# Optimization experiments

Measured on AMD Instinct MI355X. Metric: run time of the kernel, lower is better.

Reference implementation:

```python
import jax, jax.numpy as jnp
import numpy as np

HID, HEADS, FFN = 2048, 16, 8192
HEAD_DIM = HID // HEADS
B, S = 2, 2048
EPS = 1e-5


def setup_inputs() -> dict:
    key = jax.random.key(0)
    ks = jax.random.split(key, 12)
    s = 0.02
    x = jax.random.normal(ks[0], (B, S, HID), dtype=jnp.float32)
    # additive causal mask: 0 on/below diagonal, -inf-like above
    neg = jnp.float32(-1e9)
    causal = jnp.where(jnp.tril(jnp.ones((S, S), dtype=bool)), 0.0, neg)
    mask = causal[None, None, :, :].astype(jnp.float32)
    return {
        "x": x,
        "mask": mask,
        "ln1_w": jnp.ones((HID,), jnp.float32),
        "ln1_b": jnp.zeros((HID,), jnp.float32),
        "q_w": jax.random.normal(ks[1], (HID, HID), jnp.float32) * s,
        "k_w": jax.random.normal(ks[2], (HID, HID), jnp.float32) * s,
        "v_w": jax.random.normal(ks[3], (HID, HID), jnp.float32) * s,
        "o_w": jax.random.normal(ks[4], (HID, HID), jnp.float32) * s,
        "ln2_w": jnp.ones((HID,), jnp.float32),
        "ln2_b": jnp.zeros((HID,), jnp.float32),
        "w1_w": jax.random.normal(ks[5], (FFN, HID), jnp.float32) * s,
        "w1_b": jnp.zeros((FFN,), jnp.float32),
        "wg_w": jax.random.normal(ks[6], (FFN, HID), jnp.float32) * s,
        "w2_w": jax.random.normal(ks[7], (HID, FFN), jnp.float32) * s,
        "w2_b": jnp.zeros((HID,), jnp.float32),
    }


def _layernorm(x, w, b):
    mu = jnp.mean(x, axis=-1, keepdims=True)
    var = jnp.mean(jnp.square(x - mu), axis=-1, keepdims=True)
    return (x - mu) * jax.lax.rsqrt(var + EPS) * w + b


def reference(x, mask, ln1_w, ln1_b, q_w, k_w, v_w, o_w,
              ln2_w, ln2_b, w1_w, w1_b, wg_w, w2_w, w2_b):
    b, s, _ = x.shape
    # --- attention sublayer ---
    h = _layernorm(x, ln1_w, ln1_b)
    def split_heads(y):  # [b,s,hid] -> [b,H,s,d]
        return y.reshape(b, s, HEADS, HEAD_DIM).transpose(0, 2, 1, 3)
    q = split_heads(h @ q_w.T)
    k = split_heads(h @ k_w.T)
    v = split_heads(h @ v_w.T)
    scale = jnp.sqrt(jnp.float32(HEAD_DIM))
    scores = jnp.einsum('bhqd,bhkd->bhqk', q, k) / scale + mask
    weights = jax.nn.softmax(scores, axis=-1)
    attn = jnp.einsum('bhqk,bhkd->bhqd', weights, v)
    attn = attn.transpose(0, 2, 1, 3).reshape(b, s, HID)
    x = x + attn @ o_w.T
    # --- SwiGLU FFN sublayer ---
    h2 = _layernorm(x, ln2_w, ln2_b)
    ff = jax.nn.silu(h2 @ w1_w.T + w1_b) * (h2 @ wg_w.T)
    x = x + ff @ w2_w.T + w2_b
    return x
```

## Files before the change

kernel.cpp:

```cpp
#include <hip/hip_runtime.h>
#include <cstdint>
#include <cstddef>

#define HIDN 2048
#define NROWS 4096
#define FFND 8192
#define SEQ 2048

typedef __attribute__((ext_vector_type(8))) __bf16 bf16x8;
typedef __attribute__((ext_vector_type(4))) float f32x4;

__device__ __forceinline__ unsigned short f2b(float f) {
    union { float f; unsigned u; } v; v.f = f;
    unsigned r = v.u + 0x7fffu + ((v.u >> 16) & 1u);
    return (unsigned short)(r >> 16);
}
__device__ __forceinline__ float b2f(unsigned short h) {
    union { unsigned u; float f; } v; v.u = ((unsigned)h) << 16; return v.f;
}
__device__ __forceinline__ void gload16(const void* g, void* lds) {
    __builtin_amdgcn_global_load_lds(
        (const __attribute__((address_space(1))) void*)g,
        (__attribute__((address_space(3))) void*)lds, 16, 0, 0);
}

__global__ __launch_bounds__(256) void f2b_kernel(const float* __restrict__ in,
                                                  unsigned short* __restrict__ out, int n4) {
    int i = blockIdx.x * 256 + threadIdx.x;
    if (i < n4) {
        float4 v = ((const float4*)in)[i];
        ushort4 o;
        o.x = f2b(v.x); o.y = f2b(v.y); o.z = f2b(v.z); o.w = f2b(v.w);
        ((ushort4*)out)[i] = o;
    }
}

__global__ __launch_bounds__(256) void ln_kernel(const float* __restrict__ x,
                                                 const float* __restrict__ w,
                                                 const float* __restrict__ b,
                                                 unsigned short* __restrict__ out) {
    int row = blockIdx.x, tid = threadIdx.x;
    const float4* xr = (const float4*)(x + (size_t)row * HIDN);
    float4 a0 = xr[tid], a1 = xr[tid + 256];
    float s  = a0.x + a0.y + a0.z + a0.w + a1.x + a1.y + a1.z + a1.w;
    float s2 = a0.x*a0.x + a0.y*a0.y + a0.z*a0.z + a0.w*a0.w
             + a1.x*a1.x + a1.y*a1.y + a1.z*a1.z + a1.w*a1.w;
#pragma unroll
    for (int i = 1; i < 64; i <<= 1) { s += __shfl_xor(s, i); s2 += __shfl_xor(s2, i); }
    __shared__ float red[8];
    if ((tid & 63) == 0) { red[tid >> 6] = s; red[4 + (tid >> 6)] = s2; }
    __syncthreads();
    s  = red[0] + red[1] + red[2] + red[3];
    s2 = red[4] + red[5] + red[6] + red[7];
    float mu  = s * (1.0f / HIDN);
    float var = s2 * (1.0f / HIDN) - mu * mu;
    float rstd = rsqrtf(var + 1e-5f);
    const float4* wv = (const float4*)w;
    const float4* bv = (const float4*)b;
    float4 w0 = wv[tid], w1 = wv[tid + 256], b0 = bv[tid], b1 = bv[tid + 256];
    ushort4 o0, o1;
    o0.x = f2b((a0.x - mu) * rstd * w0.x + b0.x);
    o0.y = f2b((a0.y - mu) * rstd * w0.y + b0.y);
    o0.z = f2b((a0.z - mu) * rstd * w0.z + b0.z);
    o0.w = f2b((a0.w - mu) * rstd * w0.w + b0.w);
    o1.x = f2b((a1.x - mu) * rstd * w1.x + b1.x);
    o1.y = f2b((a1.y - mu) * rstd * w1.y + b1.y);
    o1.z = f2b((a1.z - mu) * rstd * w1.z + b1.z);
    o1.w = f2b((a1.w - mu) * rstd * w1.w + b1.w);
    ushort4* orow = (ushort4*)(out + (size_t)row * HIDN);
    orow[tid] = o0; orow[tid + 256] = o1;
}

template <int EPI>
__global__ __launch_bounds__(256)
void gemm_bt(const unsigned short* __restrict__ A, const unsigned short* __restrict__ Bw,
             int M, int N, int K, int tiles_n, float scale,
             const float* __restrict__ bias, const float* __restrict__ resf,
             const unsigned short* __restrict__ aux,
             float* __restrict__ outf, unsigned short* __restrict__ outb) {
    __shared__ unsigned short Asm[128 * 32];
    __shared__ unsigned short Bsm[128 * 32];
    int tid = threadIdx.x;
    int wave = tid >> 6, lane = tid & 63;
    int lrow = lane & 15, quad = lane >> 4;
    int bm = blockIdx.x / tiles_n, bn = blockIdx.x % tiles_n;
    int wm = (wave >> 1) * 64, wn = (wave & 1) * 64;

    f32x4 acc[4][4];
#pragma unroll
    for (int i = 0; i < 4; i++)
#pragma unroll
        for (int j = 0; j < 4; j++) acc[i][j] = f32x4{0.f, 0.f, 0.f, 0.f};

    int srow = wave * 32 + (lane >> 2);
    int scol = (lane & 3) * 8;
    const unsigned short* Ag = A + (size_t)(bm * 128 + srow) * K + scol;
    const unsigned short* Bg = Bw + (size_t)(bn * 128 + srow) * K + scol;
    unsigned short* AsmC0 = &Asm[(wave * 2 + 0) * 512];
    unsigned short* AsmC1 = &Asm[(wave * 2 + 1) * 512];
    unsigned short* BsmC0 = &Bsm[(wave * 2 + 0) * 512];
    unsigned short* BsmC1 = &Bsm[(wave * 2 + 1) * 512];

    for (int k0 = 0; k0 < K; k0 += 32) {
        gload16(Ag + k0, AsmC0);
        gload16(Ag + k0 + (size_t)16 * K, AsmC1);
        gload16(Bg + k0, BsmC0);
        gload16(Bg + k0 + (size_t)16 * K, BsmC1);
        __syncthreads();
        bf16x8 af[4], bfb[4];
#pragma unroll
        for (int mi = 0; mi < 4; mi++)
            af[mi] = *(const bf16x8*)&Asm[(wm + mi * 16 + lrow) * 32 + quad * 8];
#pragma unroll
        for (int ni = 0; ni < 4; ni++)
            bfb[ni] = *(const bf16x8*)&Bsm[(wn + ni * 16 + lrow) * 32 + quad * 8];
#pragma unroll
        for (int mi = 0; mi < 4; mi++)
#pragma unroll
            for (int ni = 0; ni < 4; ni++)
                acc[mi][ni] = __builtin_amdgcn_mfma_f32_16x16x32_bf16(af[mi], bfb[ni], acc[mi][ni], 0, 0, 0);
        __syncthreads();
    }

    int row0 = bm * 128 + wm, col0 = bn * 128 + wn;
#pragma unroll
    for (int mi = 0; mi < 4; mi++) {
#pragma unroll
        for (int ni = 0; ni < 4; ni++) {
            int c = col0 + ni * 16 + lrow;
#pragma unroll
            for (int r = 0; r < 4; r++) {
                int rr = row0 + mi * 16 + quad * 4 + r;
                size_t idx = (size_t)rr * N + c;
                float vv = acc[mi][ni][r];
                if constexpr (EPI == 0) {
                    outb[idx] = f2b(vv * scale);
                } else if constexpr (EPI == 1) {
                    outf[idx] = vv + resf[idx];
                } else if constexpr (EPI == 2) {
                    outb[idx] = f2b(vv + bias[c]);
                } else if constexpr (EPI == 3) {
                    float av = b2f(aux[idx]);
                    float sl = av / (1.f + __expf(-av));
                    outb[idx] = f2b(sl * vv);
                } else if constexpr (EPI == 4) {
                    outf[idx] = vv + bias[c] + resf[idx];
                }
            }
        }
    }
}

__global__ __launch_bounds__(256)
void attn_kernel(const unsigned short* __restrict__ q, const unsigned short* __restrict__ k,
                 const unsigned short* __restrict__ v, unsigned short* __restrict__ o) {
    int bh = blockIdx.x;
    int qt = 31 - blockIdx.y;
    int b = bh >> 4, h = bh & 15;
    int tid = threadIdx.x, wave = tid >> 6, lane = tid & 63;
    int lrow = lane & 15, quad = lane >> 4;
    int q0 = qt * 64;
    size_t base = ((size_t)b * SEQ) * HIDN + h * 128;

    __shared__ unsigned short Ksm[64 * 136];
    __shared__ unsigned short VTsm[128 * 72];
    __shared__ unsigned short Psm[4 * 16 * 72];

    bf16x8 qf[4];
    {
        const unsigned short* qp = q + base + (size_t)(q0 + wave * 16 + lrow) * HIDN + quad * 8;
#pragma unroll
        for (int kc = 0; kc < 4; kc++) qf[kc] = *(const bf16x8*)(qp + kc * 32);
    }

    f32x4 oacc[8];
#pragma unroll
    for (int i = 0; i < 8; i++) oacc[i] = f32x4{0.f, 0.f, 0.f, 0.f};
    float m_run[4], l_run[4];
    int rowg[4];
#pragma unroll
    for (int r = 0; r < 4; r++) {
        m_run[r] = -1e30f; l_run[r] = 0.f;
        rowg[r] = q0 + wave * 16 + quad * 4 + r;
    }

    for (int kt = 0; kt <= qt; ++kt) {
        {
            int r = tid >> 2, cc = (tid & 3) * 32;
            const uint4* src = (const uint4*)(k + base + (size_t)(kt * 64 + r) * HIDN + cc);
            uint4* dst = (uint4*)&Ksm[r * 136 + cc];
            dst[0] = src[0]; dst[1] = src[1]; dst[2] = src[2]; dst[3] = src[3];
        }
        {
            int kv = (tid >> 3) * 2, d0 = (tid & 7) * 16;
            const unsigned short* vp = v + base + (size_t)(kt * 64 + kv) * HIDN + d0;
            unsigned short va[16], vb[16];
            *(uint4*)&va[0] = ((const uint4*)vp)[0];
            *(uint4*)&va[8] = ((const uint4*)vp)[1];
            *(uint4*)&vb[0] = ((const uint4*)(vp + HIDN))[0];
            *(uint4*)&vb[8] = ((const uint4*)(vp + HIDN))[1];
#pragma unroll
            for (int i = 0; i < 16; i++) {
                unsigned pair = (unsigned)va[i] | ((unsigned)vb[i] << 16);
                *(unsigned*)&VTsm[(d0 + i) * 72 + kv] = pair;
            }
        }
        __syncthreads();

        f32x4 sacc[4];
#pragma unroll
        for (int ns = 0; ns < 4; ns++) sacc[ns] = f32x4{0.f, 0.f, 0.f, 0.f};
#pragma unroll
        for (int ns = 0; ns < 4; ns++) {
            const unsigned short* kb = &Ksm[(ns * 16 + lrow) * 136 + quad * 8];
#pragma unroll
            for (int kc = 0; kc < 4; kc++) {
                bf16x8 kf = *(const bf16x8*)(kb + kc * 32);
                sacc[ns] = __builtin_amdgcn_mfma_f32_16x16x32_bf16(qf[kc], kf, sacc[ns], 0, 0, 0);
            }
        }
#pragma unroll
        for (int ns = 0; ns < 4; ns++) {
            int colg = kt * 64 + ns * 16 + lrow;
#pragma unroll
            for (int r = 0; r < 4; r++)
                if (colg > rowg[r]) sacc[ns][r] = -1e30f;
        }
        float mnew[4], alpha[4], rsum[4];
#pragma unroll
        for (int r = 0; r < 4; r++) {
            float mv = fmaxf(fmaxf(sacc[0][r], sacc[1][r]), fmaxf(sacc[2][r], sacc[3][r]));
#pragma unroll
            for (int off = 1; off < 16; off <<= 1) mv = fmaxf(mv, __shfl_xor(mv, off));
            mnew[r] = fmaxf(m_run[r], mv);
            alpha[r] = __expf(m_run[r] - mnew[r]);
            rsum[r] = 0.f;
        }
#pragma unroll
        for (int ns = 0; ns < 4; ns++)
#pragma unroll
            for (int r = 0; r < 4; r++) {
                float p = __expf(sacc[ns][r] - mnew[r]);
                sacc[ns][r] = p;
                rsum[r] += p;
            }
#pragma unroll
        for (int r = 0; r < 4; r++) {
#pragma unroll
            for (int off = 1; off < 16; off <<= 1) rsum[r] += __shfl_xor(rsum[r], off);
            l_run[r] = l_run[r] * alpha[r] + rsum[r];
            m_run[r] = mnew[r];
        }
#pragma unroll
        for (int nc = 0; nc < 8; nc++)
#pragma unroll
            for (int r = 0; r < 4; r++) oacc[nc][r] *= alpha[r];

        unsigned short* pw = &Psm[wave * 16 * 72];
#pragma unroll
        for (int ns = 0; ns < 4; ns++)
#pragma unroll
            for (int r = 0; r < 4; r++)
                pw[(quad * 4 + r) * 72 + ns * 16 + lrow] = f2b(sacc[ns][r]);
        __syncthreads();
        bf16x8 pf[2];
#pragma unroll
        for (int kc = 0; kc < 2; kc++)
            pf[kc] = *(const bf16x8*)&pw[lrow * 72 + kc * 32 + quad * 8];
#pragma unroll
        for (int nc = 0; nc < 8; nc++) {
#pragma unroll
            for (int kc = 0; kc < 2; kc++) {
                bf16x8 vf = *(const bf16x8*)&VTsm[(nc * 16 + lrow) * 72 + kc * 32 + quad * 8];
                oacc[nc] = __builtin_amdgcn_mfma_f32_16x16x32_bf16(pf[kc], vf, oacc[nc], 0, 0, 0);
            }
        }
        __syncthreads();
    }

    float inv[4];
#pragma unroll
    for (int r = 0; r < 4; r++) inv[r] = 1.f / l_run[r];
#pragma unroll
    for (int nc = 0; nc < 8; nc++) {
#pragma unroll
        for (int r = 0; r < 4; r++) {
            int srow = q0 + wave * 16 + quad * 4 + r;
            o[base + (size_t)srow * HIDN + nc * 16 + lrow] = f2b(oacc[nc][r] * inv[r]);
        }
    }
}

extern "C" void kernel_launch(void* const* d_in, const int* in_sizes, int n_in,
                              void* d_out, int out_size, void* d_ws, size_t ws_size,
                              hipStream_t stream) {
    const float* x    = (const float*)d_in[0];
    const float* ln1w = (const float*)d_in[2];
    const float* ln1b = (const float*)d_in[3];
    const float* qw   = (const float*)d_in[4];
    const float* kw   = (const float*)d_in[5];
    const float* vw   = (const float*)d_in[6];
    const float* ow   = (const float*)d_in[7];
    const float* ln2w = (const float*)d_in[8];
    const float* ln2b = (const float*)d_in[9];
    const float* w1w  = (const float*)d_in[10];
    const float* w1bias = (const float*)d_in[11];
    const float* wgw  = (const float*)d_in[12];
    const float* w2w  = (const float*)d_in[13];
    const float* w2bias = (const float*)d_in[14];
    float* out = (float*)d_out;

    char* ws = (char*)d_ws;
    const size_t MB = 1ull << 20;
    unsigned short* qwb  = (unsigned short*)(ws + 0 * MB);
    unsigned short* kwb  = (unsigned short*)(ws + 8 * MB);
    unsigned short* vwb  = (unsigned short*)(ws + 16 * MB);
    unsigned short* owb  = (unsigned short*)(ws + 24 * MB);
    unsigned short* w1wb = (unsigned short*)(ws + 32 * MB);
    unsigned short* wgwb = (unsigned short*)(ws + 64 * MB);
    unsigned short* w2wb = (unsigned short*)(ws + 96 * MB);
    unsigned short* a1   = (unsigned short*)(ws + 128 * MB);
    unsigned short* hbuf = (unsigned short*)(ws + 128 * MB);
    unsigned short* qb   = (unsigned short*)(ws + 144 * MB);
    unsigned short* kb   = (unsigned short*)(ws + 160 * MB);
    unsigned short* vb   = (unsigned short*)(ws + 176 * MB);
    unsigned short* attnb= (unsigned short*)(ws + 192 * MB);
    unsigned short* h2   = (unsigned short*)(ws + 208 * MB);
    float*          x1   = out;

    f2b_kernel<<<4096, 256, 0, stream>>>(qw, qwb, HIDN * HIDN / 4);
    f2b_kernel<<<4096, 256, 0, stream>>>(kw, kwb, HIDN * HIDN / 4);
    f2b_kernel<<<4096, 256, 0, stream>>>(vw, vwb, HIDN * HIDN / 4);
    f2b_kernel<<<4096, 256, 0, stream>>>(ow, owb, HIDN * HIDN / 4);
    f2b_kernel<<<16384, 256, 0, stream>>>(w1w, w1wb, FFND * HIDN / 4);
    f2b_kernel<<<16384, 256, 0, stream>>>(wgw, wgwb, FFND * HIDN / 4);
    f2b_kernel<<<16384, 256, 0, stream>>>(w2w, w2wb, HIDN * FFND / 4);

    ln_kernel<<<NROWS, 256, 0, stream>>>(x, ln1w, ln1b, hbuf);

    const float qscale = 0.08838834764831845f;
    gemm_bt<0><<<dim3(32 * 16), 256, 0, stream>>>(hbuf, qwb, NROWS, HIDN, HIDN, 16, qscale,
                                                  nullptr, nullptr, nullptr, nullptr, qb);
    gemm_bt<0><<<dim3(32 * 16), 256, 0, stream>>>(hbuf, kwb, NROWS, HIDN, HIDN, 16, 1.0f,
                                                  nullptr, nullptr, nullptr, nullptr, kb);
    gemm_bt<0><<<dim3(32 * 16), 256, 0, stream>>>(hbuf, vwb, NROWS, HIDN, HIDN, 16, 1.0f,
                                                  nullptr, nullptr, nullptr, nullptr, vb);
    attn_kernel<<<dim3(32, 32), 256, 0, stream>>>(qb, kb, vb, attnb);
    gemm_bt<1><<<dim3(32 * 16), 256, 0, stream>>>(attnb, owb, NROWS, HIDN, HIDN, 16, 1.0f,
                                                  nullptr, x, nullptr, x1, nullptr);
    ln_kernel<<<NROWS, 256, 0, stream>>>(x1, ln2w, ln2b, h2);
    gemm_bt<2><<<dim3(32 * 64), 256, 0, stream>>>(h2, w1wb, NROWS, FFND, HIDN, 64, 1.0f,
                                                  w1bias, nullptr, nullptr, nullptr, a1);
    gemm_bt<3><<<dim3(32 * 64), 256, 0, stream>>>(h2, wgwb, NROWS, FFND, HIDN, 64, 1.0f,
                                                  nullptr, nullptr, a1, nullptr, a1);
    gemm_bt<4><<<dim3(32 * 16), 256, 0, stream>>>(a1, w2wb, NROWS, HIDN, FFND, 16, 1.0f,
                                                  w2bias, x1, nullptr, out, nullptr);
    (void)in_sizes; (void)n_in; (void)out_size; (void)ws_size;
}
```

Before: 1.304 ms.

## Fuse QKV projections into one GEMM and process two K-slices per barrier

The Q, K and V weight matrices are packed into one 6144-wide bf16 buffer, and a single GEMM writes an interleaved QKV activation. A new epilogue applies the query scale only to the first 2048 columns. The attention kernel now reads Q, K and V from this strided buffer. Separately, the GEMM main loop stages two 32-wide K slices into doubled LDS buffers before each barrier pair, halving barrier count per K step. Together these cut two kernel launches, give one larger grid better fill, and reduce sync overhead, at the cost of more LDS per block and strided attention loads.

```diff
diff --git a/kernel.cpp b/kernel.cpp
--- a/kernel.cpp
+++ b/kernel.cpp
@@ -6,6 +6,7 @@
 #define NROWS 4096
 #define FFND 8192
 #define SEQ 2048
+#define QKVN 6144
 
 typedef __attribute__((ext_vector_type(8))) __bf16 bf16x8;
 typedef __attribute__((ext_vector_type(4))) float f32x4;
@@ -78,8 +79,8 @@
              const float* __restrict__ bias, const float* __restrict__ resf,
              const unsigned short* __restrict__ aux,
              float* __restrict__ outf, unsigned short* __restrict__ outb) {
-    __shared__ unsigned short Asm[128 * 32];
-    __shared__ unsigned short Bsm[128 * 32];
+    __shared__ unsigned short Asm[2][128 * 32];
+    __shared__ unsigned short Bsm[2][128 * 32];
     int tid = threadIdx.x;
     int wave = tid >> 6, lane = tid & 63;
     int lrow = lane & 15, quad = lane >> 4;
@@ -96,29 +97,31 @@
     int scol = (lane & 3) * 8;
     const unsigned short* Ag = A + (size_t)(bm * 128 + srow) * K + scol;
     const unsigned short* Bg = Bw + (size_t)(bn * 128 + srow) * K + scol;
-    unsigned short* AsmC0 = &Asm[(wave * 2 + 0) * 512];
-    unsigned short* AsmC1 = &Asm[(wave * 2 + 1) * 512];
-    unsigned short* BsmC0 = &Bsm[(wave * 2 + 0) * 512];
-    unsigned short* BsmC1 = &Bsm[(wave * 2 + 1) * 512];
-
-    for (int k0 = 0; k0 < K; k0 += 32) {
-        gload16(Ag + k0, AsmC0);
-        gload16(Ag + k0 + (size_t)16 * K, AsmC1);
-        gload16(Bg + k0, BsmC0);
-        gload16(Bg + k0 + (size_t)16 * K, BsmC1);
-        __syncthreads();
-        bf16x8 af[4], bfb[4];
-#pragma unroll
-        for (int mi = 0; mi < 4; mi++)
-            af[mi] = *(const bf16x8*)&Asm[(wm + mi * 16 + lrow) * 32 + quad * 8];
-#pragma unroll
-        for (int ni = 0; ni < 4; ni++)
-            bfb[ni] = *(const bf16x8*)&Bsm[(wn + ni * 16 + lrow) * 32 + quad * 8];
-#pragma unroll
-        for (int mi = 0; mi < 4; mi++)
+
+    for (int k0 = 0; k0 < K; k0 += 64) {
+#pragma unroll
+        for (int s = 0; s < 2; s++) {
+            gload16(Ag + k0 + s * 32, &Asm[s][(wave * 2 + 0) * 512]);
+            gload16(Ag + k0 + s * 32 + (size_t)16 * K, &Asm[s][(wave * 2 + 1) * 512]);
+            gload16(Bg + k0 + s * 32, &Bsm[s][(wave * 2 + 0) * 512]);
+            gload16(Bg + k0 + s * 32 + (size_t)16 * K, &Bsm[s][(wave * 2 + 1) * 512]);
+        }
+        __syncthreads();
+#pragma unroll
+        for (int s = 0; s < 2; s++) {
+            bf16x8 af[4], bfb[4];
+#pragma unroll
+            for (int mi = 0; mi < 4; mi++)
+                af[mi] = *(const bf16x8*)&Asm[s][(wm + mi * 16 + lrow) * 32 + quad * 8];
 #pragma unroll
             for (int ni = 0; ni < 4; ni++)
-                acc[mi][ni] = __builtin_amdgcn_mfma_f32_16x16x32_bf16(af[mi], bfb[ni], acc[mi][ni], 0, 0, 0);
+                bfb[ni] = *(const bf16x8*)&Bsm[s][(wn + ni * 16 + lrow) * 32 + quad * 8];
+#pragma unroll
+            for (int mi = 0; mi < 4; mi++)
+#pragma unroll
+                for (int ni = 0; ni < 4; ni++)
+                    acc[mi][ni] = __builtin_amdgcn_mfma_f32_16x16x32_bf16(af[mi], bfb[ni], acc[mi][ni], 0, 0, 0);
+        }
         __syncthreads();
     }
 
@@ -145,6 +148,8 @@
                     outb[idx] = f2b(sl * vv);
                 } else if constexpr (EPI == 4) {
                     outf[idx] = vv + bias[c] + resf[idx];
+                } else if constexpr (EPI == 5) {
+                    outb[idx] = f2b(vv * (c < HIDN ? scale : 1.0f));
                 }
             }
         }
@@ -152,15 +157,18 @@
 }
 
 __global__ __launch_bounds__(256)
-void attn_kernel(const unsigned short* __restrict__ q, const unsigned short* __restrict__ k,
-                 const unsigned short* __restrict__ v, unsigned short* __restrict__ o) {
+void attn_kernel(const unsigned short* __restrict__ qkv, unsigned short* __restrict__ o) {
     int bh = blockIdx.x;
     int qt = 31 - blockIdx.y;
     int b = bh >> 4, h = bh & 15;
     int tid = threadIdx.x, wave = tid >> 6, lane = tid & 63;
     int lrow = lane & 15, quad = lane >> 4;
     int q0 = qt * 64;
-    size_t base = ((size_t)b * SEQ) * HIDN + h * 128;
+    size_t base = ((size_t)b * SEQ) * QKVN + h * 128;
+    const unsigned short* qp0 = qkv + base;
+    const unsigned short* kp0 = qkv + base + HIDN;
+    const unsigned short* vp0 = qkv + base + 2 * HIDN;
+    size_t obase = ((size_t)b * SEQ) * HIDN + h * 128;
 
     __shared__ unsigned short Ksm[64 * 136];
     __shared__ unsigned short VTsm[128 * 72];
@@ -168,7 +176,7 @@
 
     bf16x8 qf[4];
     {
-        const unsigned short* qp = q + base + (size_t)(q0 + wave * 16 + lrow) * HIDN + quad * 8;
+        const unsigned short* qp = qp0 + (size_t)(q0 + wave * 16 + lrow) * QKVN + quad * 8;
 #pragma unroll
         for (int kc = 0; kc < 4; kc++) qf[kc] = *(const bf16x8*)(qp + kc * 32);
     }
@@ -187,18 +195,18 @@
     for (int kt = 0; kt <= qt; ++kt) {
         {
             int r = tid >> 2, cc = (tid & 3) * 32;
-            const uint4* src = (const uint4*)(k + base + (size_t)(kt * 64 + r) * HIDN + cc);
+            const uint4* src = (const uint4*)(kp0 + (size_t)(kt * 64 + r) * QKVN + cc);
             uint4* dst = (uint4*)&Ksm[r * 136 + cc];
             dst[0] = src[0]; dst[1] = src[1]; dst[2] = src[2]; dst[3] = src[3];
         }
         {
             int kv = (tid >> 3) * 2, d0 = (tid & 7) * 16;
-            const unsigned short* vp = v + base + (size_t)(kt * 64 + kv) * HIDN + d0;
+            const unsigned short* vp = vp0 + (size_t)(kt * 64 + kv) * QKVN + d0;
             unsigned short va[16], vb[16];
             *(uint4*)&va[0] = ((const uint4*)vp)[0];
             *(uint4*)&va[8] = ((const uint4*)vp)[1];
-            *(uint4*)&vb[0] = ((const uint4*)(vp + HIDN))[0];
-            *(uint4*)&vb[8] = ((const uint4*)(vp + HIDN))[1];
+            *(uint4*)&vb[0] = ((const uint4*)(vp + QKVN))[0];
+            *(uint4*)&vb[8] = ((const uint4*)(vp + QKVN))[1];
 #pragma unroll
             for (int i = 0; i < 16; i++) {
                 unsigned pair = (unsigned)va[i] | ((unsigned)vb[i] << 16);
@@ -286,7 +294,7 @@
 #pragma unroll
         for (int r = 0; r < 4; r++) {
             int srow = q0 + wave * 16 + quad * 4 + r;
-            o[base + (size_t)srow * HIDN + nc * 16 + lrow] = f2b(oacc[nc][r] * inv[r]);
+            o[obase + (size_t)srow * HIDN + nc * 16 + lrow] = f2b(oacc[nc][r] * inv[r]);
         }
     }
 }
@@ -312,25 +320,21 @@
 
     char* ws = (char*)d_ws;
     const size_t MB = 1ull << 20;
-    unsigned short* qwb  = (unsigned short*)(ws + 0 * MB);
-    unsigned short* kwb  = (unsigned short*)(ws + 8 * MB);
-    unsigned short* vwb  = (unsigned short*)(ws + 16 * MB);
+    unsigned short* qkvwb = (unsigned short*)(ws + 0 * MB);
     unsigned short* owb  = (unsigned short*)(ws + 24 * MB);
     unsigned short* w1wb = (unsigned short*)(ws + 32 * MB);
     unsigned short* wgwb = (unsigned short*)(ws + 64 * MB);
     unsigned short* w2wb = (unsigned short*)(ws + 96 * MB);
     unsigned short* a1   = (unsigned short*)(ws + 128 * MB);
     unsigned short* hbuf = (unsigned short*)(ws + 128 * MB);
-    unsigned short* qb   = (unsigned short*)(ws + 144 * MB);
-    unsigned short* kb   = (unsigned short*)(ws + 160 * MB);
-    unsigned short* vb   = (unsigned short*)(ws + 176 * MB);
+    unsigned short* qkvb = (unsigned short*)(ws + 144 * MB);
     unsigned short* attnb= (unsigned short*)(ws + 192 * MB);
     unsigned short* h2   = (unsigned short*)(ws + 208 * MB);
     float*          x1   = out;
 
-    f2b_kernel<<<4096, 256, 0, stream>>>(qw, qwb, HIDN * HIDN / 4);
-    f2b_kernel<<<4096, 256, 0, stream>>>(kw, kwb, HIDN * HIDN / 4);
-    f2b_kernel<<<4096, 256, 0, stream>>>(vw, vwb, HIDN * HIDN / 4);
+    f2b_kernel<<<4096, 256, 0, stream>>>(qw, qkvwb, HIDN * HIDN / 4);
+    f2b_kernel<<<4096, 256, 0, stream>>>(kw, qkvwb + (size_t)HIDN * HIDN, HIDN * HIDN / 4);
+    f2b_kernel<<<4096, 256, 0, stream>>>(vw, qkvwb + (size_t)2 * HIDN * HIDN, HIDN * HIDN / 4);
     f2b_kernel<<<4096, 256, 0, stream>>>(ow, owb, HIDN * HIDN / 4);
     f2b_kernel<<<16384, 256, 0, stream>>>(w1w, w1wb, FFND * HIDN / 4);
     f2b_kernel<<<16384, 256, 0, stream>>>(wgw, wgwb, FFND * HIDN / 4);
@@ -339,13 +343,9 @@
     ln_kernel<<<NROWS, 256, 0, stream>>>(x, ln1w, ln1b, hbuf);
 
     const float qscale = 0.08838834764831845f;
-    gemm_bt<0><<<dim3(32 * 16), 256, 0, stream>>>(hbuf, qwb, NROWS, HIDN, HIDN, 16, qscale,
-                                                  nullptr, nullptr, nullptr, nullptr, qb);
-    gemm_bt<0><<<dim3(32 * 16), 256, 0, stream>>>(hbuf, kwb, NROWS, HIDN, HIDN, 16, 1.0f,
-                                                  nullptr, nullptr, nullptr, nullptr, kb);
-    gemm_bt<0><<<dim3(32 * 16), 256, 0, stream>>>(hbuf, vwb, NROWS, HIDN, HIDN, 16, 1.0f,
-                                                  nullptr, nullptr, nullptr, nullptr, vb);
-    attn_kernel<<<dim3(32, 32), 256, 0, stream>>>(qb, kb, vb, attnb);
+    gemm_bt<5><<<dim3(32 * 48), 256, 0, stream>>>(hbuf, qkvwb, NROWS, QKVN, HIDN, 48, qscale,
+                                                  nullptr, nullptr, nullptr, nullptr, qkvb);
+    attn_kernel<<<dim3(32, 32), 256, 0, stream>>>(qkvb, attnb);
     gemm_bt<1><<<dim3(32 * 16), 256, 0, stream>>>(attnb, owb, NROWS, HIDN, HIDN, 16, 1.0f,
                                                   nullptr, x, nullptr, x1, nullptr);
     ln_kernel<<<NROWS, 256, 0, stream>>>(x1, ln2w, ln2b, h2);
```

Result: faster. 1.191 ms (-8.7%).
